# Optimization experiments

Hardware: AMD Instinct MI355X
Metric: run time of the kernel (lower is better)

The kernel has to match this reference:

```python
import jax, jax.numpy as jnp
import numpy as np

B, T, H = 4096, 8, 512


def setup_inputs() -> dict:
    key = jax.random.key(0)
    ks = jax.random.split(key, 14)
    s = 1.0 / np.sqrt(H)
    u = lambda k, shape: jax.random.uniform(k, shape, jnp.float32, -s, s)
    return {
        "inps": jax.random.normal(ks[0], (B, T, H), jnp.float32),
        "enc_output": jax.random.normal(ks[1], (B, T, H), jnp.float32),
        "conv_w": u(ks[2], (1, T, 1)),   # Conv1d(tuple_len,1,1) weight
        "conv_b": u(ks[3], (1,)),
        "Wih": u(ks[4], (4 * H, H)),      # LSTM input weights (i,f,g,o)
        "Whh": u(ks[5], (4 * H, H)),
        "bih": u(ks[6], (4 * H,)),
        "bhh": u(ks[7], (4 * H,)),
        "W1": u(ks[8], (H, H)),           # attn.W1
        "b1": u(ks[9], (H,)),
        "W2": u(ks[10], (H, H)),          # attn.W2
        "b2": u(ks[11], (H,)),
        "vw": u(ks[12], (1, H)),          # attn.v
        "vb": u(ks[13], (1,)),
    }


def reference(inps, enc_output, conv_w, conv_b, Wih, Whh, bih, bhh, W1, b1, W2, b2, vw, vb):
    Bv, Tv, Hv = enc_output.shape
    # Conv1d(tuple_len -> 1, kernel 1): mix over the tuple (channel) dim
    inp0 = jnp.einsum('bch,c->bh', enc_output, conv_w[0, :, 0]) + conv_b[0]  # [B,H]
    # W1 @ E is step-invariant: hoist out of the decode loop (same math)
    W1E = jnp.einsum('bth,oh->bto', enc_output, W1) + b1  # [B,T,H]
    bidx = jnp.arange(Bv)

    def step(carry, _):
        h, c, mask, inp = carry
        # single-layer LSTM cell, torch gate order i,f,g,o
        gates = inp @ Wih.T + bih + h @ Whh.T + bhh  # [B,4H]
        i_, f_, g_, o_ = jnp.split(gates, 4, axis=-1)
        c = jax.nn.sigmoid(f_) * c + jax.nn.sigmoid(i_) * jnp.tanh(g_)
        h = jax.nn.sigmoid(o_) * jnp.tanh(c)  # di
        # additive attention: v(tanh(W1 E + W2 di))
        Ui = jnp.einsum('bth,h->bt', jnp.tanh(W1E + (h @ W2.T + b2)[:, None, :]), vw[0]) + vb[0]
        ai = jax.nn.softmax(Ui, axis=1)
        ai = jnp.where(mask, -jnp.inf, ai)  # masking happens AFTER softmax, as in source
        ptr = jnp.argmax(ai, axis=1)  # [B]
        mask = mask.at[bidx, ptr].set(True)
        inp = inps[bidx, ptr]  # gather next decoder input
        return (h, c, mask, inp), (Ui, ptr)

    h0 = jnp.zeros((Bv, Hv), inps.dtype)
    c0 = jnp.zeros_like(h0)
    mask0 = jnp.zeros((Bv, Tv), dtype=bool)
    # first torch step uses mask=None, equivalent to an all-False mask -> uniform scan
    _, (Uis, ptrs) = jax.lax.scan(step, (h0, c0, mask0, inp0), None, length=Tv)
    probs = jnp.transpose(Uis, (1, 0, 2))  # [B, T, T]
    ptrs = jnp.transpose(ptrs, (1, 0))     # [B, T]
    return probs, ptrs
```

## Files before the change

kernel.cpp:

```cpp
#include <hip/hip_runtime.h>
#include <hip/hip_bf16.h>

#define Bn 4096
#define Tn 8
#define Hn 512

typedef __attribute__((ext_vector_type(8))) _Float16 half8v;
typedef __attribute__((ext_vector_type(4))) float f32x4;

__device__ __forceinline__ float sigm(float x) { return 0.5f * tanhf(0.5f * x) + 0.5f; }

__device__ __forceinline__ short f2h(float x) {
    _Float16 h = (_Float16)x;
    return *reinterpret_cast<short*>(&h);
}
__device__ __forceinline__ float h2f(short s) {
    _Float16 h = *reinterpret_cast<_Float16*>(&s);
    return (float)h;
}
__device__ __forceinline__ void split2(float x, short& hi, short& lo) {
    hi = f2h(x);
    lo = f2h((x - h2f(hi)) * 4096.0f);
}

#define GLOAD16(g, l) __builtin_amdgcn_global_load_lds( \
    (const __attribute__((address_space(1))) unsigned int*)(g), \
    (__attribute__((address_space(3))) unsigned int*)(l), 16, 0, 0)


__global__ __launch_bounds__(256) void k_prep(const float* __restrict__ Wih,
                                              const float* __restrict__ Whh,
                                              const float* __restrict__ bih,
                                              const float* __restrict__ bhh,
                                              short* __restrict__ WcatHi,
                                              short* __restrict__ WcatLo,
                                              float* __restrict__ bcat) {
    int tid = blockIdx.x * 256 + threadIdx.x;
    int jp = tid >> 10, k = tid & 1023;
    int g = (jp >> 4) & 3;
    int h = (jp & 15) + ((jp >> 6) << 4);
    int j = g * 512 + h;
    float v = (k < 512) ? Wih[j * 512 + k] : Whh[j * 512 + (k - 512)];
    short hi, lo; split2(v, hi, lo);
    WcatHi[tid] = hi; WcatLo[tid] = lo;
    if (k == 0) bcat[jp] = bih[j] + bhh[j];
}

__global__ __launch_bounds__(256) void k_split4(const float* __restrict__ x,
                                                short* __restrict__ hi,
                                                short* __restrict__ lo, int n4) {
    int i = blockIdx.x * 256 + threadIdx.x;
    if (i >= n4) return;
    float4 v = ((const float4*)x)[i];
    short h0, l0, h1, l1, h2, l2, h3, l3;
    split2(v.x, h0, l0); split2(v.y, h1, l1);
    split2(v.z, h2, l2); split2(v.w, h3, l3);
    ((short4*)hi)[i] = make_short4(h0, h1, h2, h3);
    ((short4*)lo)[i] = make_short4(l0, l1, l2, l3);
}

__global__ __launch_bounds__(256) void k_init(const float* __restrict__ enc,
                                              const float* __restrict__ cw,
                                              const float* __restrict__ cb,
                                              short* __restrict__ Xhi,
                                              short* __restrict__ Xlo,
                                              float* __restrict__ C,
                                              int* __restrict__ mask) {
    int tid = blockIdx.x * 256 + threadIdx.x;
    int b = tid >> 9, h = tid & 511;
    float s = cb[0];
    const float* e = enc + ((size_t)b << 12) + h;
#pragma unroll
    for (int t = 0; t < Tn; ++t) s = fmaf(e[t * Hn], cw[t], s);
    short hi, lo; split2(s, hi, lo);
    size_t xb = ((size_t)b << 10) + h;
    Xhi[xb] = hi; Xlo[xb] = lo;
    Xhi[xb + 512] = 0; Xlo[xb + 512] = 0;
    C[tid] = 0.0f;
    if (h == 0) mask[b] = 0;
}

template <int NW, bool FUSE, int SWZ>
__global__ __launch_bounds__(512) void gemm_t(
    const short* __restrict__ Ahi, const short* __restrict__ Alo, int lda,
    const short* __restrict__ Whi, const short* __restrict__ Wlo,
    const float* __restrict__ bias, float* __restrict__ out,
    float* __restrict__ Cst, short* __restrict__ Xh, short* __restrict__ Xl,
    int N, int K) {
    constexpr int BN = 32 * NW;
    constexpr int NJ = NW;
    constexpr int BUFSH = 8192 + 2 * BN * 32;
    __shared__ short sm[2 * BUFSH];

    int bx = blockIdx.x, by = blockIdx.y;
    if constexpr (SWZ == 1) {
        int w = bx + (by << 4), c = w & 7, k = w >> 3;
        by = ((c >> 1) << 3) | (k >> 3);
        bx = ((c & 1) << 3) | (k & 7);
    } else if constexpr (SWZ == 2) {
        int w = bx + (by << 2), c = w & 7, k = w >> 3;
        by = (c << 5) | (k >> 2);
        bx = k & 3;
    } else if constexpr (SWZ == 3) {
        int w = bx + (by << 3), c = w & 7, k = w >> 3;
        by = ((c >> 1) << 3) | (k >> 2);
        bx = ((c & 1) << 2) | (k & 3);
    }

    const int tid = threadIdx.x;
    const int lane = tid & 63;
    const int wv = tid >> 6;
    const int wm = wv >> 1;
    const int wn = wv & 1;
    const int lm = lane & 15, lk = lane >> 4;
    const int m0 = by * 128, n0 = bx * BN;

    f32x4 acc[2][NJ] = {};
    f32x4 acc2[2][NJ] = {};

    float bb[NJ];
#pragma unroll
    for (int j = 0; j < NJ; ++j) bb[j] = bias[n0 + wn * (BN >> 1) + j * 16 + lm];

    auto STAGE = [&](int buf, int k0) {
        short* base = sm + buf * BUFSH;
        {
            int row = tid >> 2, sq = tid & 3;
            int qg = sq ^ ((row >> 1) & 3);
            size_t aoff = (size_t)(m0 + row) * lda + k0 + qg * 8;
            GLOAD16(Ahi + aoff, base + tid * 8);
            GLOAD16(Alo + aoff, base + 4096 + tid * 8);
        }
        if (BN == 128 || tid < BN * 4) {
            int row = tid >> 2, sq = tid & 3;
            int qg = sq ^ ((row >> 1) & 3);
            size_t boff = (size_t)(n0 + row) * K + k0 + qg * 8;
            GLOAD16(Whi + boff, base + 8192 + tid * 8);
            GLOAD16(Wlo + boff, base + 8192 + BN * 32 + tid * 8);
        }
    };

    STAGE(0, 0);
    int cur = 0;
    for (int k0 = 0; k0 < K; k0 += 32) {
        __syncthreads();
        if (k0 + 32 < K) STAGE(cur ^ 1, k0 + 32);

        short* base = sm + cur * BUFSH;
        half8v ahi[2], alo[2], bhi[NJ], blo[NJ];
#pragma unroll
        for (int i = 0; i < 2; ++i) {
            int ra = wm * 32 + i * 16 + lm;
            int offa = ra * 32 + (lk ^ ((ra >> 1) & 3)) * 8;
            ahi[i] = *(const half8v*)&base[offa];
            alo[i] = *(const half8v*)&base[4096 + offa];
        }
#pragma unroll
        for (int j = 0; j < NJ; ++j) {
            int rb = wn * (BN >> 1) + j * 16 + lm;
            int offb = rb * 32 + (lk ^ ((rb >> 1) & 3)) * 8;
            bhi[j] = *(const half8v*)&base[8192 + offb];
            blo[j] = *(const half8v*)&base[8192 + BN * 32 + offb];
        }
#pragma unroll
        for (int i = 0; i < 2; ++i)
#pragma unroll
            for (int j = 0; j < NJ; ++j) {
                acc[i][j]  = __builtin_amdgcn_mfma_f32_16x16x32_f16(ahi[i], bhi[j], acc[i][j], 0, 0, 0);
                acc2[i][j] = __builtin_amdgcn_mfma_f32_16x16x32_f16(ahi[i], blo[j], acc2[i][j], 0, 0, 0);
                acc2[i][j] = __builtin_amdgcn_mfma_f32_16x16x32_f16(alo[i], bhi[j], acc2[i][j], 0, 0, 0);
            }
        cur ^= 1;
    }

    const float ls = 1.0f / 4096.0f;

    if constexpr (FUSE) {
        const int h = lm + 16 * ((n0 >> 6) + wn);
#pragma unroll
        for (int i = 0; i < 2; ++i) {
#pragma unroll
            for (int r = 0; r < 4; ++r) {
                int brow = m0 + wm * 32 + i * 16 + lk * 4 + r;
                float gi = acc[i][0][r] + ls * acc2[i][0][r] + bb[0];
                float gf = acc[i][1][r] + ls * acc2[i][1][r] + bb[1];
                float gg = acc[i][2][r] + ls * acc2[i][2][r] + bb[2];
                float go = acc[i][3][r] + ls * acc2[i][3][r] + bb[3];
                size_t ch = ((size_t)brow << 9) + h;
                float c = sigm(gf) * Cst[ch] + sigm(gi) * tanhf(gg);
                float hn = sigm(go) * tanhf(c);
                Cst[ch] = c;
                short shi, slo; split2(hn, shi, slo);
                size_t xb = ((size_t)brow << 10) + 512 + h;
                Xh[xb] = shi; Xl[xb] = slo;
            }
        }
    } else {
        __syncthreads();
        constexpr int SW = 16 * NJ + 4;
        float* tile = reinterpret_cast<float*>(sm) + wv * 16 * SW;
        constexpr int LPR = 4 * NJ;
        const int rl = lane / LPR, cc = lane % LPR;
#pragma unroll
        for (int i = 0; i < 2; ++i) {
#pragma unroll
            for (int j = 0; j < NJ; ++j)
#pragma unroll
                for (int r = 0; r < 4; ++r)
                    tile[(lk * 4 + r) * SW + j * 16 + lm] = acc[i][j][r] + ls * acc2[i][j][r] + bb[j];
            constexpr int RPS = 64 / LPR;
#pragma unroll
            for (int s = 0; s < 16 / RPS; ++s) {
                int row = s * RPS + rl;
                float4 v = *(float4*)&tile[row * SW + cc * 4];
                *(float4*)(out + (size_t)(m0 + wm * 32 + i * 16 + row) * N +
                           n0 + wn * (BN >> 1) + cc * 4) = v;
            }
        }
    }
}

__global__ __launch_bounds__(256) void k_attn(const float* __restrict__ W1E,
                                              const float* __restrict__ W2h,
                                              const float* __restrict__ vw,
                                              const float* __restrict__ vbp,
                                              const float* __restrict__ inps,
                                              short* __restrict__ Xhi,
                                              short* __restrict__ Xlo,
                                              int* __restrict__ mask,
                                              float* __restrict__ probs,
                                              float* __restrict__ ptrs,
                                              int step) {
    const int b = blockIdx.x;
    const int tid = threadIdx.x;
    const int lane = tid & 63;
    const int wv = tid >> 6;
    __shared__ float sU[Tn];
    __shared__ int sptr;

    const float4* w2p = (const float4*)(W2h + (size_t)b * Hn + lane * 8);
    float4 w2a = w2p[0], w2b = w2p[1];
    const float4* vp = (const float4*)(vw + lane * 8);
    float4 va = vp[0], vb4 = vp[1];
    float vbias = vbp[0];

#pragma unroll
    for (int q = 0; q < 2; ++q) {
        int t = wv * 2 + q;
        const float4* w1 = (const float4*)(W1E + ((size_t)b << 12) + t * Hn + lane * 8);
        float4 u0 = w1[0], u1 = w1[1];
        float p = va.x * tanhf(u0.x + w2a.x) + va.y * tanhf(u0.y + w2a.y)
                + va.z * tanhf(u0.z + w2a.z) + va.w * tanhf(u0.w + w2a.w)
                + vb4.x * tanhf(u1.x + w2b.x) + vb4.y * tanhf(u1.y + w2b.y)
                + vb4.z * tanhf(u1.z + w2b.z) + vb4.w * tanhf(u1.w + w2b.w);
#pragma unroll
        for (int off = 32; off; off >>= 1) p += __shfl_down(p, off, 64);
        if (lane == 0) sU[t] = p + vbias;
    }
    __syncthreads();

    if (tid == 0) {
        int mk = mask[b];
        float best = -1e30f;
        int ptr = 0;
#pragma unroll
        for (int t = 0; t < Tn; ++t) {
            probs[(size_t)b * 64 + step * 8 + t] = sU[t];
            if (!((mk >> t) & 1) && sU[t] > best) { best = sU[t]; ptr = t; }
        }
        mask[b] = mk | (1 << ptr);
        ptrs[(size_t)b * 8 + step] = (float)ptr;
        sptr = ptr;
    }
    __syncthreads();
    const float2* src = (const float2*)(inps + ((size_t)b << 12) + (size_t)sptr * Hn);
    float2 v = src[tid];
    short h0, l0, h1, l1;
    split2(v.x, h0, l0); split2(v.y, h1, l1);
    size_t xb = ((size_t)b << 10) + tid * 2;
    *(short2*)&Xhi[xb] = make_short2(h0, h1);
    *(short2*)&Xlo[xb] = make_short2(l0, l1);
}

extern "C" void kernel_launch(void* const* d_in, const int* in_sizes, int n_in,
                              void* d_out, int out_size, void* d_ws, size_t ws_size,
                              hipStream_t stream) {
    const float* inps  = (const float*)d_in[0];
    const float* enc   = (const float*)d_in[1];
    const float* convw = (const float*)d_in[2];
    const float* convb = (const float*)d_in[3];
    const float* Wih   = (const float*)d_in[4];
    const float* Whh   = (const float*)d_in[5];
    const float* bih   = (const float*)d_in[6];
    const float* bhh   = (const float*)d_in[7];
    const float* W1    = (const float*)d_in[8];
    const float* b1    = (const float*)d_in[9];
    const float* W2    = (const float*)d_in[10];
    const float* b2    = (const float*)d_in[11];
    const float* vw    = (const float*)d_in[12];
    const float* vb    = (const float*)d_in[13];

    float* out   = (float*)d_out;
    float* probs = out;
    float* ptrs  = out + (size_t)Bn * 64;

    char* wsb = (char*)d_ws;
    float* W1E    = (float*)wsb;
    short* encHi  = (short*)(wsb + (64ull << 20));
    short* encLo  = (short*)(wsb + (96ull << 20));
    short* Xhi1   = (short*)(wsb + (64ull << 20));
    short* Xlo1   = (short*)(wsb + (72ull << 20));
    float* W2h    = (float*)(wsb + (96ull << 20));
    float* C      = (float*)(wsb + (104ull << 20));
    short* Xhi0   = (short*)(wsb + (112ull << 20));
    short* Xlo0   = (short*)(wsb + (120ull << 20));
    short* WcatHi = (short*)(wsb + (128ull << 20));
    short* WcatLo = (short*)(wsb + (132ull << 20));
    short* W1hi   = (short*)(wsb + (136ull << 20));
    short* W1lo   = (short*)(wsb + (136ull << 20) + (512u << 10));
    short* W2hi   = (short*)(wsb + (137ull << 20));
    short* W2lo   = (short*)(wsb + (137ull << 20) + (512u << 10));
    float* bcat   = (float*)(wsb + (138ull << 20));
    int*   mask   = (int*)(wsb + (138ull << 20) + (16u << 10));

    k_prep<<<(2048 * 1024) / 256, 256, 0, stream>>>(Wih, Whh, bih, bhh, WcatHi, WcatLo, bcat);
    k_split4<<<(Bn * Tn * Hn / 4) / 256, 256, 0, stream>>>(enc, encHi, encLo, Bn * Tn * Hn / 4);
    k_split4<<<(Hn * Hn / 4) / 256, 256, 0, stream>>>(W1, W1hi, W1lo, Hn * Hn / 4);
    k_split4<<<(Hn * Hn / 4) / 256, 256, 0, stream>>>(W2, W2hi, W2lo, Hn * Hn / 4);

    gemm_t<4, false, 2><<<dim3(Hn / 128, (Bn * Tn) / 128), 512, 0, stream>>>(
        encHi, encLo, Hn, W1hi, W1lo, b1, W1E, nullptr, nullptr, nullptr, Hn, Hn);

    k_init<<<(Bn * Hn) / 256, 256, 0, stream>>>(enc, convw, convb, Xhi0, Xlo0, C, mask);

    for (int step = 0; step < Tn; ++step) {
        short* Xh_cur = (step & 1) ? Xhi1 : Xhi0;
        short* Xl_cur = (step & 1) ? Xlo1 : Xlo0;
        short* Xh_nxt = (step & 1) ? Xhi0 : Xhi1;
        short* Xl_nxt = (step & 1) ? Xlo0 : Xlo1;

        gemm_t<4, true, 1><<<dim3(2048 / 128, Bn / 128), 512, 0, stream>>>(
            Xh_cur, Xl_cur, 1024, WcatHi, WcatLo, bcat, nullptr, C, Xh_nxt, Xl_nxt, 2048, 1024);
        gemm_t<2, false, 3><<<dim3(Hn / 64, Bn / 128), 512, 0, stream>>>(
            Xh_nxt + 512, Xl_nxt + 512, 1024, W2hi, W2lo, b2, W2h, nullptr, nullptr, nullptr, Hn, Hn);
        k_attn<<<Bn, 256, 0, stream>>>(W1E, W2h, vw, vb, inps, Xh_nxt, Xl_nxt, mask, probs, ptrs, step);
    }
}
```

Baseline: 879.4 us.

## Deepen GEMM global-to-LDS pipeline with explicit vmcnt waits and two-stage prefetch

Restructures the split-fp16 MFMA GEMM main loop so it issues prefetches two k-tiles ahead into the double buffer. It uses explicit s_waitcnt vmcnt counts and raw s_barrier in place of __syncthreads, and the next stage's loads are issued right after the LDS fragment reads complete, so more global load latency overlaps with MFMA work. For the 8-wave configuration, B-tile staging is spread so each thread issues one load (hi or lo) rather than two. The risk is correctness if the vmcnt counts do not match the number of outstanding loads per thread, plus an added barrier per iteration.

```diff
diff --git a/kernel.cpp b/kernel.cpp
--- a/kernel.cpp
+++ b/kernel.cpp
@@ -131,20 +131,39 @@
             GLOAD16(Ahi + aoff, base + tid * 8);
             GLOAD16(Alo + aoff, base + 4096 + tid * 8);
         }
-        if (BN == 128 || tid < BN * 4) {
+        if constexpr (NW == 4) {
             int row = tid >> 2, sq = tid & 3;
             int qg = sq ^ ((row >> 1) & 3);
             size_t boff = (size_t)(n0 + row) * K + k0 + qg * 8;
             GLOAD16(Whi + boff, base + 8192 + tid * 8);
             GLOAD16(Wlo + boff, base + 8192 + BN * 32 + tid * 8);
+        } else {
+            int t2 = tid & 255;
+            int row = t2 >> 2, sq = t2 & 3;
+            int qg = sq ^ ((row >> 1) & 3);
+            size_t boff = (size_t)(n0 + row) * K + k0 + qg * 8;
+            const short* src = (tid < 256) ? (Whi + boff) : (Wlo + boff);
+            short* dst = base + 8192 + ((tid < 256) ? 0 : BN * 32) + t2 * 8;
+            GLOAD16(src, dst);
         }
     };
 
+    const int nkt = K >> 5;
+    asm volatile("s_waitcnt vmcnt(0)" ::: "memory");
+    __builtin_amdgcn_sched_barrier(0);
     STAGE(0, 0);
-    int cur = 0;
-    for (int k0 = 0; k0 < K; k0 += 32) {
-        __syncthreads();
-        if (k0 + 32 < K) STAGE(cur ^ 1, k0 + 32);
+    STAGE(1, 32);
+
+    for (int kt = 0; kt < nkt; ++kt) {
+        const int cur = kt & 1;
+        if (kt == nkt - 1) {
+            asm volatile("s_waitcnt vmcnt(0)" ::: "memory");
+        } else {
+            if constexpr (NW == 4) asm volatile("s_waitcnt vmcnt(4)" ::: "memory");
+            else                   asm volatile("s_waitcnt vmcnt(3)" ::: "memory");
+        }
+        __builtin_amdgcn_s_barrier();
+        __builtin_amdgcn_sched_barrier(0);
 
         short* base = sm + cur * BUFSH;
         half8v ahi[2], alo[2], bhi[NJ], blo[NJ];
@@ -162,6 +181,12 @@
             bhi[j] = *(const half8v*)&base[8192 + offb];
             blo[j] = *(const half8v*)&base[8192 + BN * 32 + offb];
         }
+        asm volatile("s_waitcnt lgkmcnt(0)" ::: "memory");
+        __builtin_amdgcn_sched_barrier(0);
+        __builtin_amdgcn_s_barrier();
+        __builtin_amdgcn_sched_barrier(0);
+        if (kt + 2 < nkt) STAGE(cur, (kt + 2) * 32);
+
 #pragma unroll
         for (int i = 0; i < 2; ++i)
 #pragma unroll
@@ -170,7 +195,6 @@
                 acc2[i][j] = __builtin_amdgcn_mfma_f32_16x16x32_f16(ahi[i], blo[j], acc2[i][j], 0, 0, 0);
                 acc2[i][j] = __builtin_amdgcn_mfma_f32_16x16x32_f16(alo[i], bhi[j], acc2[i][j], 0, 0, 0);
             }
-        cur ^= 1;
     }
 
     const float ls = 1.0f / 4096.0f;
```

Result: no change. 873.4 us (-0.7%).
